# Optimization experiments

Hardware: AMD Instinct MI355X
Metric: run time of the kernel (lower is better)

Reference implementation:

```python
import jax, jax.numpy as jnp
import numpy as np

B, S, E, H = 2, 2048, 1024, 16
HD = E // H


def setup_inputs() -> dict:
    key = jax.random.key(0)
    k1, k2, k3, k4 = jax.random.split(key, 4)
    x = jax.random.normal(k1, (B, S, E), dtype=jnp.float32)
    # nn.Linear(E, 3E, bias=False): weight shape (3E, E), y = x @ W.T
    w_qkv = jax.random.normal(k2, (3 * E, E), dtype=jnp.float32) * (E ** -0.5)
    w_proj = jax.random.normal(k3, (E, E), dtype=jnp.float32) * (E ** -0.5)
    b_proj = jax.random.normal(k4, (E,), dtype=jnp.float32) * 0.02
    return {"x": x, "w_qkv": w_qkv, "w_proj": w_proj, "b_proj": b_proj}


def reference(x, w_qkv, w_proj, b_proj):
    b, s, e = x.shape
    hd = e // H
    qkv = x @ w_qkv.T                                   # (B,S,3E)
    qkv = qkv.reshape(b, s, H, 3, hd)                   # matches view(B,S,H,3*hd).chunk(3,-1)
    q = jnp.transpose(qkv[..., 0, :], (0, 2, 1, 3))      # (B,H,S,hd)
    k = jnp.transpose(qkv[..., 1, :], (0, 2, 1, 3))
    v = jnp.transpose(qkv[..., 2, :], (0, 2, 1, 3))
    scale = hd ** -0.5
    scores = jnp.einsum('bhqd,bhkd->bhqk', q, k) * scale  # (B,H,S,S)
    causal = jnp.tril(jnp.ones((s, s), dtype=bool))
    scores = jnp.where(causal, scores, jnp.float32(-jnp.inf))
    probs = jax.nn.softmax(scores, axis=-1)
    out = jnp.einsum('bhqk,bhkd->bhqd', probs, v)        # (B,H,S,hd)
    out = jnp.transpose(out, (0, 2, 1, 3)).reshape(b, s, e)
    return out @ w_proj.T + b_proj
```

## Files before the change

### kernel.cpp

```cpp
#include <hip/hip_runtime.h>
#include <hip/hip_bf16.h>

#define B_    2
#define S_    2048
#define E_    1024
#define H_    16
#define HD_   64
#define M_    (B_ * S_)
#define QKVN  (3 * E_)

typedef __attribute__((ext_vector_type(8))) short  short8;
typedef __attribute__((ext_vector_type(4))) float  f32x4;
typedef __attribute__((ext_vector_type(4))) unsigned short us16x4;

static __device__ __forceinline__ unsigned short f2bf(float f) {
  union { float f; unsigned int u; } c; c.f = f;
  unsigned int u = c.u;
  return (unsigned short)((u + 0x7fffu + ((u >> 16) & 1u)) >> 16);
}

static __device__ __forceinline__ void gload16(unsigned short* lds,
                                               const unsigned short* g) {
  __builtin_amdgcn_global_load_lds(
      (__attribute__((address_space(1))) void*)g,
      (__attribute__((address_space(3))) void*)lds, 16, 0, 0);
}

__global__ __launch_bounds__(256) void cvt_f32_to_bf16(
    const float* __restrict__ in, unsigned short* __restrict__ out, int n4) {
  int i = blockIdx.x * 256 + threadIdx.x;
  if (i < n4) {
    float4 v = reinterpret_cast<const float4*>(in)[i];
    ushort4 r;
    r.x = f2bf(v.x); r.y = f2bf(v.y); r.z = f2bf(v.z); r.w = f2bf(v.w);
    reinterpret_cast<ushort4*>(out)[i] = r;
  }
}

template <int BF16_OUT, int BN>
__global__ __launch_bounds__(256) void gemm_bt(
    const unsigned short* __restrict__ A, const unsigned short* __restrict__ Bt,
    void* __restrict__ Cout, const float* __restrict__ bias,
    int M, int N, int K, int ldc) {
  constexpr int NF = BN / 32;
  __shared__ alignas(16) unsigned short lds_a[128 * 64];
  __shared__ alignas(16) unsigned short lds_b[BN * 64];
  const int t  = threadIdx.x;
  const int w  = t >> 6, l = t & 63, g = l >> 4, lr = l & 15;
  const int bm = blockIdx.y * 128, bn = blockIdx.x * BN;
  const int wr = (w >> 1) * 64,  wc = (w & 1) * (BN / 2);

  f32x4 acc[4][NF] = {};

  for (int k0 = 0; k0 < K; k0 += 64) {
    __syncthreads();
#pragma unroll
    for (int i = 0; i < 4; i++) {
      const int pass = w * 4 + i;
      const int r = pass * 8 + (l >> 3);
      const int c = (l & 7) ^ (r & 7);
      gload16(lds_a + pass * 512, A + (size_t)(bm + r) * K + k0 + c * 8);
    }
#pragma unroll
    for (int i = 0; i < NF; i++) {
      const int pass = w * NF + i;
      const int r = pass * 8 + (l >> 3);
      const int c = (l & 7) ^ (r & 7);
      gload16(lds_b + pass * 512, Bt + (size_t)(bn + r) * K + k0 + c * 8);
    }
    __syncthreads();

    short8 af[4][2], bfr[NF][2];
#pragma unroll
    for (int m = 0; m < 4; m++) {
      const int R = wr + m * 16 + lr;
#pragma unroll
      for (int kk = 0; kk < 2; kk++)
        af[m][kk] = *(const short8*)((const char*)lds_a +
            ((R * 128 + kk * 64 + g * 16) ^ ((R & 7) << 4)));
    }
#pragma unroll
    for (int n = 0; n < NF; n++) {
      const int R = wc + n * 16 + lr;
#pragma unroll
      for (int kk = 0; kk < 2; kk++)
        bfr[n][kk] = *(const short8*)((const char*)lds_b +
            ((R * 128 + kk * 64 + g * 16) ^ ((R & 7) << 4)));
    }
#pragma unroll
    for (int m = 0; m < 4; m++)
#pragma unroll
      for (int n = 0; n < NF; n++) {
        acc[m][n] = __builtin_amdgcn_mfma_f32_16x16x32_bf16(
            af[m][0], bfr[n][0], acc[m][n], 0, 0, 0);
        acc[m][n] = __builtin_amdgcn_mfma_f32_16x16x32_bf16(
            af[m][1], bfr[n][1], acc[m][n], 0, 0, 0);
      }
  }

#pragma unroll
  for (int m = 0; m < 4; m++)
#pragma unroll
    for (int n = 0; n < NF; n++)
#pragma unroll
      for (int j = 0; j < 4; j++) {
        const int row = bm + wr + m * 16 + g * 4 + j;
        const int col = bn + wc + n * 16 + lr;
        const float v = acc[m][n][j];
        if constexpr (BF16_OUT) {
          ((unsigned short*)Cout)[(size_t)row * ldc + col] = f2bf(v);
        } else {
          ((float*)Cout)[(size_t)row * ldc + col] = v + bias[col];
        }
      }
}

__global__ __launch_bounds__(256) void gemm_qkv(
    const unsigned short* __restrict__ A, const unsigned short* __restrict__ Bt,
    unsigned short* __restrict__ q_bf, unsigned short* __restrict__ k_bf,
    unsigned short* __restrict__ vt_bf, int K) {
  __shared__ alignas(16) unsigned short lds_a[128 * 64];
  __shared__ alignas(16) unsigned short lds_b[128 * 64];
  const int t  = threadIdx.x;
  const int w  = t >> 6, l = t & 63, g = l >> 4, lr = l & 15;
  const int bm = blockIdx.y * 128, bn = blockIdx.x * 128;
  const int wr = (w >> 1) * 64,  wc = (w & 1) * 64;

  f32x4 acc[4][4] = {};

  for (int k0 = 0; k0 < K; k0 += 64) {
    __syncthreads();
#pragma unroll
    for (int i = 0; i < 4; i++) {
      const int pass = w * 4 + i;
      const int r = pass * 8 + (l >> 3);
      const int c = (l & 7) ^ (r & 7);
      gload16(lds_a + pass * 512, A + (size_t)(bm + r) * K + k0 + c * 8);
      gload16(lds_b + pass * 512, Bt + (size_t)(bn + r) * K + k0 + c * 8);
    }
    __syncthreads();

    short8 af[4][2], bfr[4][2];
#pragma unroll
    for (int m = 0; m < 4; m++) {
      const int R = wr + m * 16 + lr;
#pragma unroll
      for (int kk = 0; kk < 2; kk++)
        af[m][kk] = *(const short8*)((const char*)lds_a +
            ((R * 128 + kk * 64 + g * 16) ^ ((R & 7) << 4)));
    }
#pragma unroll
    for (int n = 0; n < 4; n++) {
      const int R = wc + n * 16 + lr;
#pragma unroll
      for (int kk = 0; kk < 2; kk++)
        bfr[n][kk] = *(const short8*)((const char*)lds_b +
            ((R * 128 + kk * 64 + g * 16) ^ ((R & 7) << 4)));
    }
#pragma unroll
    for (int m = 0; m < 4; m++)
#pragma unroll
      for (int n = 0; n < 4; n++) {
        acc[m][n] = __builtin_amdgcn_mfma_f32_16x16x32_bf16(
            af[m][0], bfr[n][0], acc[m][n], 0, 0, 0);
        acc[m][n] = __builtin_amdgcn_mfma_f32_16x16x32_bf16(
            af[m][1], bfr[n][1], acc[m][n], 0, 0, 0);
      }
  }

  const int b = bm >> 11;
#pragma unroll
  for (int n = 0; n < 4; n++) {
    const int col0  = bn + wc + n * 16;
    const int hcls  = col0 / 192;
    const int cls   = (col0 % 192) / 64;
    const int cbase = col0 & 63;
    if (cls == 2) {
      const int d  = cbase + lr;
      const int sl = (bm & 2047) + wr + g * 4;
#pragma unroll
      for (int m = 0; m < 4; m++) {
        us16x4 pk;
#pragma unroll
        for (int j = 0; j < 4; j++) pk[j] = f2bf(acc[m][n][j]);
        *(us16x4*)(vt_bf +
            ((size_t)((b * H_ + hcls) * 64 + d) * S_ + sl + m * 16)) = pk;
      }
    } else {
      unsigned short* dst = (cls == 0) ? q_bf : k_bf;
      const int col = hcls * 64 + cbase + lr;
#pragma unroll
      for (int m = 0; m < 4; m++)
#pragma unroll
        for (int j = 0; j < 4; j++) {
          const int row = bm + wr + m * 16 + g * 4 + j;
          dst[(size_t)row * E_ + col] = f2bf(acc[m][n][j]);
        }
    }
  }
}

__global__ __launch_bounds__(256) void attn_fwd(
    const unsigned short* __restrict__ q_bf,
    const unsigned short* __restrict__ k_bf,
    const unsigned short* __restrict__ vt_bf,
    unsigned short* __restrict__ attn_out) {
  __shared__ alignas(16) unsigned short lds_k[64 * 64];
  __shared__ alignas(16) unsigned short lds_vt[64 * 64];
  __shared__ alignas(16) unsigned short lds_p[4][32 * 64];

  const int t = threadIdx.x;
  const int w = t >> 6, l = t & 63, g = (l >> 4) & 3, lr = l & 15;
  const int bid = blockIdx.x;
  const int bh = bid & 31, b = bh >> 4, h = bh & 15;
  const int rr = bid >> 5;
  const int bx = (rr < 8) ? rr : 23 - rr;
  const int q0 = bx * 128;
  const int qw = q0 + w * 32;
  const unsigned short* qbase = q_bf + (size_t)b * S_ * E_ + h * HD_;
  const unsigned short* kbase = k_bf + (size_t)b * S_ * E_ + h * HD_;
  const unsigned short* vbase = vt_bf + (size_t)(b * H_ + h) * 64 * S_;

  short8 qf[2][2];
#pragma unroll
  for (int m = 0; m < 2; m++) {
    const unsigned short* qp = qbase + (size_t)(qw + m * 16 + lr) * E_ + g * 8;
    qf[m][0] = *(const short8*)qp;
    qf[m][1] = *(const short8*)(qp + 32);
  }

  f32x4 o[2][4] = {};
  float m_r[2] = {-3.0e38f, -3.0e38f};
  float l_r[2] = {0.f, 0.f};
  const float SCALE2 = 0.18033688011112042f;

  const int numt = 2 * bx + 2;
  const int r_st = t >> 3;
  const int kc   = t & 7;

  short8 kreg[2], vreg[2];
#pragma unroll
  for (int p = 0; p < 2; p++) {
    const int r = p * 32 + r_st;
    kreg[p] = *(const short8*)(kbase + (size_t)r * E_ + kc * 8);
    vreg[p] = *(const short8*)(vbase + (size_t)r * S_ + kc * 8);
  }

  for (int kt = 0; kt < numt; kt++) {
    const int k0 = kt * 64;
#pragma unroll
    for (int p = 0; p < 2; p++) {
      const int r = p * 32 + r_st;
      const int off = (r * 128 + kc * 16) ^ ((r & 7) << 4);
      *(short8*)((char*)lds_k + off)  = kreg[p];
      *(short8*)((char*)lds_vt + off) = vreg[p];
    }
    if (kt + 1 < numt) {
#pragma unroll
      for (int p = 0; p < 2; p++) {
        const int r = p * 32 + r_st;
        kreg[p] = *(const short8*)(kbase + (size_t)(k0 + 64 + r) * E_ + kc * 8);
        vreg[p] = *(const short8*)(vbase + (size_t)r * S_ + k0 + 64 + kc * 8);
      }
    }
    __syncthreads();

    if (k0 <= qw + 31) {
      f32x4 st[2][4];
      __builtin_amdgcn_s_setprio(1);
#pragma unroll
      for (int n = 0; n < 4; n++) {
        const int R = n * 16 + lr;
        const int sw = (R & 7) << 4;
        short8 kf0 = *(const short8*)((const char*)lds_k +
            ((R * 128 + g * 16) ^ sw));
        short8 kf1 = *(const short8*)((const char*)lds_k +
            ((R * 128 + 64 + g * 16) ^ sw));
#pragma unroll
        for (int m = 0; m < 2; m++) {
          f32x4 z = {};
          z = __builtin_amdgcn_mfma_f32_16x16x32_bf16(kf0, qf[m][0], z, 0, 0, 0);
          z = __builtin_amdgcn_mfma_f32_16x16x32_bf16(kf1, qf[m][1], z, 0, 0, 0);
          st[m][n] = z;
        }
      }
      __builtin_amdgcn_s_setprio(0);

      const bool diag = (k0 + 63 > qw);

#pragma unroll
      for (int m = 0; m < 2; m++) {
        const int qrow = qw + m * 16 + lr;
        if (diag) {
#pragma unroll
          for (int n = 0; n < 4; n++)
#pragma unroll
            for (int j = 0; j < 4; j++)
              if ((k0 + n * 16 + g * 4 + j) > qrow) st[m][n][j] = -3.0e38f;
        }
        float mx = st[m][0][0];
#pragma unroll
        for (int n = 0; n < 4; n++)
#pragma unroll
          for (int j = 0; j < 4; j++) mx = fmaxf(mx, st[m][n][j]);
        mx = fmaxf(mx, __shfl_xor(mx, 16, 64));
        mx = fmaxf(mx, __shfl_xor(mx, 32, 64));
        const float mn = fmaxf(m_r[m], mx * SCALE2);
        const float c  = exp2f(m_r[m] - mn);
        m_r[m] = mn;
        float p[4][4];
        float sum = 0.f;
#pragma unroll
        for (int n = 0; n < 4; n++)
#pragma unroll
          for (int j = 0; j < 4; j++) {
            p[n][j] = exp2f(fmaf(st[m][n][j], SCALE2, -mn));
            sum += p[n][j];
          }
        sum += __shfl_xor(sum, 16, 64);
        sum += __shfl_xor(sum, 32, 64);
        l_r[m] = l_r[m] * c + sum;
#pragma unroll
        for (int dt = 0; dt < 4; dt++) o[m][dt] *= c;
        char* pb = (char*)lds_p[w];
        const int rowb = (m * 16 + lr) * 128;
        const int sw   = (lr & 7) << 4;
#pragma unroll
        for (int n = 0; n < 4; n++) {
          unsigned w0, w1;
          __asm__("v_cvt_pk_bf16_f32 %0, %1, %2"
                  : "=v"(w0) : "v"(p[n][0]), "v"(p[n][1]));
          __asm__("v_cvt_pk_bf16_f32 %0, %1, %2"
                  : "=v"(w1) : "v"(p[n][2]), "v"(p[n][3]));
          uint2 val; val.x = w0; val.y = w1;
          *(uint2*)(pb + ((rowb + n * 32 + g * 8) ^ sw)) = val;
        }
      }
      __asm__ volatile("s_waitcnt lgkmcnt(0)" ::: "memory");

      short8 pf[2][2];
#pragma unroll
      for (int m = 0; m < 2; m++) {
        const int rowb = (m * 16 + lr) * 128;
        const int sw   = (lr & 7) << 4;
        pf[m][0] = *(const short8*)((const char*)lds_p[w] +
            ((rowb + g * 16) ^ sw));
        pf[m][1] = *(const short8*)((const char*)lds_p[w] +
            ((rowb + 64 + g * 16) ^ sw));
      }
      __builtin_amdgcn_s_setprio(1);
#pragma unroll
      for (int dt = 0; dt < 4; dt++) {
        const int R = dt * 16 + lr;
        const int sw = (R & 7) << 4;
        short8 vf0 = *(const short8*)((const char*)lds_vt +
            ((R * 128 + g * 16) ^ sw));
        short8 vf1 = *(const short8*)((const char*)lds_vt +
            ((R * 128 + 64 + g * 16) ^ sw));
#pragma unroll
        for (int m = 0; m < 2; m++) {
          o[m][dt] = __builtin_amdgcn_mfma_f32_16x16x32_bf16(
              vf0, pf[m][0], o[m][dt], 0, 0, 0);
          o[m][dt] = __builtin_amdgcn_mfma_f32_16x16x32_bf16(
              vf1, pf[m][1], o[m][dt], 0, 0, 0);
        }
      }
      __builtin_amdgcn_s_setprio(0);
    }

    __syncthreads();
  }

  unsigned short* outp = attn_out + (size_t)b * S_ * E_ + h * HD_;
#pragma unroll
  for (int m = 0; m < 2; m++) {
    const float inv = 1.0f / l_r[m];
    const int qrow = qw + m * 16 + lr;
#pragma unroll
    for (int dt = 0; dt < 4; dt++) {
      us16x4 w4;
#pragma unroll
      for (int j = 0; j < 4; j++) w4[j] = f2bf(o[m][dt][j] * inv);
      *(us16x4*)(outp + (size_t)qrow * E_ + dt * 16 + g * 4) = w4;
    }
  }
}

extern "C" void kernel_launch(void* const* d_in, const int* in_sizes, int n_in,
                              void* d_out, int out_size, void* d_ws, size_t ws_size,
                              hipStream_t stream) {
  (void)in_sizes; (void)n_in; (void)out_size; (void)ws_size;
  const float* x      = (const float*)d_in[0];
  const float* w_qkv  = (const float*)d_in[1];
  const float* w_proj = (const float*)d_in[2];
  const float* b_proj = (const float*)d_in[3];
  float* out = (float*)d_out;

  unsigned short* x_bf     = (unsigned short*)d_ws;
  unsigned short* wqkv_bf  = x_bf    + (size_t)M_ * E_;
  unsigned short* wproj_bf = wqkv_bf + (size_t)QKVN * E_;
  unsigned short* q_bf     = wproj_bf + (size_t)E_ * E_;
  unsigned short* k_bf     = q_bf    + (size_t)M_ * E_;
  unsigned short* vt_bf    = k_bf    + (size_t)M_ * E_;
  unsigned short* attn_bf  = vt_bf   + (size_t)M_ * E_;

  int n4;
  n4 = M_ * E_ / 4;
  cvt_f32_to_bf16<<<(n4 + 255) / 256, 256, 0, stream>>>(x, x_bf, n4);
  n4 = QKVN * E_ / 4;
  cvt_f32_to_bf16<<<(n4 + 255) / 256, 256, 0, stream>>>(w_qkv, wqkv_bf, n4);
  n4 = E_ * E_ / 4;
  cvt_f32_to_bf16<<<(n4 + 255) / 256, 256, 0, stream>>>(w_proj, wproj_bf, n4);

  gemm_qkv<<<dim3(QKVN / 128, M_ / 128), 256, 0, stream>>>(
      x_bf, wqkv_bf, q_bf, k_bf, vt_bf, E_);

  attn_fwd<<<dim3(512), 256, 0, stream>>>(q_bf, k_bf, vt_bf, attn_bf);

  gemm_bt<0, 64><<<dim3(E_ / 64, M_ / 128), 256, 0, stream>>>(
      attn_bf, wproj_bf, (void*)out, b_proj, M_, E_, E_, E_);
}
```

Measured before the change: 215.4 us.

## Load K/V fragments directly from global per warp, drop LDS staging and barriers

Each warp now loads its K and V^T MFMA fragments straight from global memory into registers instead of staging shared 64x64 tiles in LDS behind block-wide __syncthreads. Each warp runs its own tile count so it stops at its causal limit rather than idling. Also adds a lazy rescale that skips the online-softmax correction unless the max grows by more than 8 (log2 units), and sets launch bounds to 2 blocks per CU. The trade is that the four warps no longer share K/V loads through LDS, so global/L2 traffic rises and register pressure grows.

```diff
diff --git a/kernel.cpp b/kernel.cpp
--- a/kernel.cpp
+++ b/kernel.cpp
@@ -200,13 +200,11 @@
   }
 }
 
-__global__ __launch_bounds__(256) void attn_fwd(
+__global__ __launch_bounds__(256, 2) void attn_fwd(
     const unsigned short* __restrict__ q_bf,
     const unsigned short* __restrict__ k_bf,
     const unsigned short* __restrict__ vt_bf,
     unsigned short* __restrict__ attn_out) {
-  __shared__ alignas(16) unsigned short lds_k[64 * 64];
-  __shared__ alignas(16) unsigned short lds_vt[64 * 64];
   __shared__ alignas(16) unsigned short lds_p[4][32 * 64];
 
   const int t = threadIdx.x;
@@ -234,141 +232,125 @@
   float l_r[2] = {0.f, 0.f};
   const float SCALE2 = 0.18033688011112042f;
 
-  const int numt = 2 * bx + 2;
-  const int r_st = t >> 3;
-  const int kc   = t & 7;
-
-  short8 kreg[2], vreg[2];
-#pragma unroll
-  for (int p = 0; p < 2; p++) {
-    const int r = p * 32 + r_st;
-    kreg[p] = *(const short8*)(kbase + (size_t)r * E_ + kc * 8);
-    vreg[p] = *(const short8*)(vbase + (size_t)r * S_ + kc * 8);
+  const int numt = (qw >> 6) + 1;
+
+  short8 kf[4][2];
+#pragma unroll
+  for (int n = 0; n < 4; n++) {
+    const unsigned short* kp = kbase + (size_t)(n * 16 + lr) * E_ + g * 8;
+    kf[n][0] = *(const short8*)kp;
+    kf[n][1] = *(const short8*)(kp + 32);
   }
 
   for (int kt = 0; kt < numt; kt++) {
     const int k0 = kt * 64;
-#pragma unroll
-    for (int p = 0; p < 2; p++) {
-      const int r = p * 32 + r_st;
-      const int off = (r * 128 + kc * 16) ^ ((r & 7) << 4);
-      *(short8*)((char*)lds_k + off)  = kreg[p];
-      *(short8*)((char*)lds_vt + off) = vreg[p];
+
+    f32x4 st[2][4];
+    __builtin_amdgcn_s_setprio(1);
+#pragma unroll
+    for (int n = 0; n < 4; n++)
+#pragma unroll
+      for (int m = 0; m < 2; m++) {
+        f32x4 z = {};
+        z = __builtin_amdgcn_mfma_f32_16x16x32_bf16(kf[n][0], qf[m][0], z, 0, 0, 0);
+        z = __builtin_amdgcn_mfma_f32_16x16x32_bf16(kf[n][1], qf[m][1], z, 0, 0, 0);
+        st[m][n] = z;
+      }
+    __builtin_amdgcn_s_setprio(0);
+
+    short8 vf[4][2];
+#pragma unroll
+    for (int dt = 0; dt < 4; dt++) {
+      const unsigned short* vp = vbase + (size_t)(dt * 16 + lr) * S_ + k0 + g * 8;
+      vf[dt][0] = *(const short8*)vp;
+      vf[dt][1] = *(const short8*)(vp + 32);
     }
     if (kt + 1 < numt) {
 #pragma unroll
-      for (int p = 0; p < 2; p++) {
-        const int r = p * 32 + r_st;
-        kreg[p] = *(const short8*)(kbase + (size_t)(k0 + 64 + r) * E_ + kc * 8);
-        vreg[p] = *(const short8*)(vbase + (size_t)r * S_ + k0 + 64 + kc * 8);
-      }
-    }
-    __syncthreads();
-
-    if (k0 <= qw + 31) {
-      f32x4 st[2][4];
-      __builtin_amdgcn_s_setprio(1);
-#pragma unroll
       for (int n = 0; n < 4; n++) {
-        const int R = n * 16 + lr;
-        const int sw = (R & 7) << 4;
-        short8 kf0 = *(const short8*)((const char*)lds_k +
-            ((R * 128 + g * 16) ^ sw));
-        short8 kf1 = *(const short8*)((const char*)lds_k +
-            ((R * 128 + 64 + g * 16) ^ sw));
-#pragma unroll
-        for (int m = 0; m < 2; m++) {
-          f32x4 z = {};
-          z = __builtin_amdgcn_mfma_f32_16x16x32_bf16(kf0, qf[m][0], z, 0, 0, 0);
-          z = __builtin_amdgcn_mfma_f32_16x16x32_bf16(kf1, qf[m][1], z, 0, 0, 0);
-          st[m][n] = z;
-        }
-      }
-      __builtin_amdgcn_s_setprio(0);
-
-      const bool diag = (k0 + 63 > qw);
-
-#pragma unroll
-      for (int m = 0; m < 2; m++) {
-        const int qrow = qw + m * 16 + lr;
-        if (diag) {
-#pragma unroll
-          for (int n = 0; n < 4; n++)
-#pragma unroll
-            for (int j = 0; j < 4; j++)
-              if ((k0 + n * 16 + g * 4 + j) > qrow) st[m][n][j] = -3.0e38f;
-        }
-        float mx = st[m][0][0];
+        const unsigned short* kp =
+            kbase + (size_t)(k0 + 64 + n * 16 + lr) * E_ + g * 8;
+        kf[n][0] = *(const short8*)kp;
+        kf[n][1] = *(const short8*)(kp + 32);
+      }
+    }
+
+    const bool diag = (k0 + 63 > qw);
+
+#pragma unroll
+    for (int m = 0; m < 2; m++) {
+      const int qrow = qw + m * 16 + lr;
+      if (diag) {
 #pragma unroll
         for (int n = 0; n < 4; n++)
 #pragma unroll
-          for (int j = 0; j < 4; j++) mx = fmaxf(mx, st[m][n][j]);
-        mx = fmaxf(mx, __shfl_xor(mx, 16, 64));
-        mx = fmaxf(mx, __shfl_xor(mx, 32, 64));
-        const float mn = fmaxf(m_r[m], mx * SCALE2);
+          for (int j = 0; j < 4; j++)
+            if ((k0 + n * 16 + g * 4 + j) > qrow) st[m][n][j] = -3.0e38f;
+      }
+      float mxn[4];
+#pragma unroll
+      for (int n = 0; n < 4; n++)
+        mxn[n] = fmaxf(fmaxf(st[m][n][0], st[m][n][1]),
+                       fmaxf(st[m][n][2], st[m][n][3]));
+      float mx = fmaxf(fmaxf(mxn[0], mxn[1]), fmaxf(mxn[2], mxn[3]));
+      mx = fmaxf(mx, __shfl_xor(mx, 16, 64));
+      mx = fmaxf(mx, __shfl_xor(mx, 32, 64));
+      const float pm = mx * SCALE2;
+      if (!__all(pm <= m_r[m] + 8.0f)) {
+        const float mn = fmaxf(m_r[m], pm);
         const float c  = exp2f(m_r[m] - mn);
         m_r[m] = mn;
-        float p[4][4];
-        float sum = 0.f;
-#pragma unroll
-        for (int n = 0; n < 4; n++)
-#pragma unroll
-          for (int j = 0; j < 4; j++) {
-            p[n][j] = exp2f(fmaf(st[m][n][j], SCALE2, -mn));
-            sum += p[n][j];
-          }
-        sum += __shfl_xor(sum, 16, 64);
-        sum += __shfl_xor(sum, 32, 64);
-        l_r[m] = l_r[m] * c + sum;
+        l_r[m] *= c;
 #pragma unroll
         for (int dt = 0; dt < 4; dt++) o[m][dt] *= c;
-        char* pb = (char*)lds_p[w];
-        const int rowb = (m * 16 + lr) * 128;
-        const int sw   = (lr & 7) << 4;
-#pragma unroll
-        for (int n = 0; n < 4; n++) {
-          unsigned w0, w1;
-          __asm__("v_cvt_pk_bf16_f32 %0, %1, %2"
-                  : "=v"(w0) : "v"(p[n][0]), "v"(p[n][1]));
-          __asm__("v_cvt_pk_bf16_f32 %0, %1, %2"
-                  : "=v"(w1) : "v"(p[n][2]), "v"(p[n][3]));
-          uint2 val; val.x = w0; val.y = w1;
-          *(uint2*)(pb + ((rowb + n * 32 + g * 8) ^ sw)) = val;
-        }
-      }
-      __asm__ volatile("s_waitcnt lgkmcnt(0)" ::: "memory");
-
-      short8 pf[2][2];
+      }
+      float p[4][4], sn[4];
+#pragma unroll
+      for (int n = 0; n < 4; n++) {
+#pragma unroll
+        for (int j = 0; j < 4; j++)
+          p[n][j] = exp2f(fmaf(st[m][n][j], SCALE2, -m_r[m]));
+        sn[n] = (p[n][0] + p[n][1]) + (p[n][2] + p[n][3]);
+      }
+      float sum = (sn[0] + sn[1]) + (sn[2] + sn[3]);
+      sum += __shfl_xor(sum, 16, 64);
+      sum += __shfl_xor(sum, 32, 64);
+      l_r[m] += sum;
+      char* pb = (char*)lds_p[w];
+      const int rowb = (m * 16 + lr) * 128;
+      const int sw   = (lr & 7) << 4;
+#pragma unroll
+      for (int n = 0; n < 4; n++) {
+        unsigned w0, w1;
+        __asm__("v_cvt_pk_bf16_f32 %0, %1, %2"
+                : "=v"(w0) : "v"(p[n][0]), "v"(p[n][1]));
+        __asm__("v_cvt_pk_bf16_f32 %0, %1, %2"
+                : "=v"(w1) : "v"(p[n][2]), "v"(p[n][3]));
+        uint2 val; val.x = w0; val.y = w1;
+        *(uint2*)(pb + ((rowb + n * 32 + g * 8) ^ sw)) = val;
+      }
+    }
+    __asm__ volatile("s_waitcnt lgkmcnt(0)" ::: "memory");
+
+    short8 pf[2][2];
+#pragma unroll
+    for (int m = 0; m < 2; m++) {
+      const int rowb = (m * 16 + lr) * 128;
+      const int sw   = (lr & 7) << 4;
+      pf[m][0] = *(const short8*)((const char*)lds_p[w] + ((rowb + g * 16) ^ sw));
+      pf[m][1] = *(const short8*)((const char*)lds_p[w] + ((rowb + 64 + g * 16) ^ sw));
+    }
+    __builtin_amdgcn_s_setprio(1);
+#pragma unroll
+    for (int dt = 0; dt < 4; dt++)
 #pragma unroll
       for (int m = 0; m < 2; m++) {
-        const int rowb = (m * 16 + lr) * 128;
-        const int sw   = (lr & 7) << 4;
-        pf[m][0] = *(const short8*)((const char*)lds_p[w] +
-            ((rowb + g * 16) ^ sw));
-        pf[m][1] = *(const short8*)((const char*)lds_p[w] +
-            ((rowb + 64 + g * 16) ^ sw));
-      }
-      __builtin_amdgcn_s_setprio(1);
-#pragma unroll
-      for (int dt = 0; dt < 4; dt++) {
-        const int R = dt * 16 + lr;
-        const int sw = (R & 7) << 4;
-        short8 vf0 = *(const short8*)((const char*)lds_vt +
-            ((R * 128 + g * 16) ^ sw));
-        short8 vf1 = *(const short8*)((const char*)lds_vt +
-            ((R * 128 + 64 + g * 16) ^ sw));
-#pragma unroll
-        for (int m = 0; m < 2; m++) {
-          o[m][dt] = __builtin_amdgcn_mfma_f32_16x16x32_bf16(
-              vf0, pf[m][0], o[m][dt], 0, 0, 0);
-          o[m][dt] = __builtin_amdgcn_mfma_f32_16x16x32_bf16(
-              vf1, pf[m][1], o[m][dt], 0, 0, 0);
-        }
-      }
-      __builtin_amdgcn_s_setprio(0);
-    }
-
-    __syncthreads();
+        o[m][dt] = __builtin_amdgcn_mfma_f32_16x16x32_bf16(
+            vf[dt][0], pf[m][0], o[m][dt], 0, 0, 0);
+        o[m][dt] = __builtin_amdgcn_mfma_f32_16x16x32_bf16(
+            vf[dt][1], pf[m][1], o[m][dt], 0, 0, 0);
+      }
+    __builtin_amdgcn_s_setprio(0);
   }
 
   unsigned short* outp = attn_out + (size_t)b * S_ * E_ + h * HD_;
```

Result: faster. 209.0 us (-3.0%).
